# Kernel tuning notes

Hardware: AMD Instinct MI355X
Metric: run time of the kernel (lower is better)

## Reference

```python
import jax, jax.numpy as jnp
import numpy as np

B, T, CIN, CH, M, NCLS = 2048, 8, 2048, 1024, 32, 21
EPS = 1e-8  # torch.cosine_similarity eps


def setup_inputs() -> dict:
    key = jax.random.key(0)
    ks = jax.random.split(key, 16)
    g = lambda k, shp, sc=0.02: jax.random.normal(k, shp, dtype=jnp.float32) * sc
    return {
        "x": g(ks[0], (B, T, CIN), 1.0),
        "static_feat": g(ks[1], (NCLS, CIN, M), 1.0),  # 21 kmeans exemplar banks
        "Wk": g(ks[2], (CH, CIN)), "bk": g(ks[3], (CH,)),
        "Wv": g(ks[4], (CH, CIN)), "bv": g(ks[5], (CH,)),
        "WEk": g(ks[6], (CH, CIN)), "bEk": g(ks[7], (CH,)),
        "WEv": g(ks[8], (CH, CIN)), "bEv": g(ks[9], (CH,)),
        "Ww": g(ks[10], (1, CH)), "bw": g(ks[11], (1,)),
        "Wout": g(ks[12], (NCLS, 2 * CH)), "bout": g(ks[13], (NCLS,)),
    }


def reference(x, static_feat, Wk, bk, Wv, bv, WEk, bEk, WEv, bEv, Ww, bw, Wout, bout):
    # last frame only: [B, CIN]
    xl = x[:, -1, :]
    # 1x1 convs on length-1 sequence == dense projections
    k = xl @ Wk.T + bk          # [B, CH]
    v = xl @ Wv.T + bv          # [B, CH]
    # project all 21 static memories at once: [NCLS, CH, M]
    Ek = jnp.einsum('oc,ncm->nom', WEk, static_feat) + bEk[None, :, None]
    Ev = jnp.einsum('oc,ncm->nom', WEv, static_feat) + bEv[None, :, None]
    # cosine similarity along channel dim (torch clamps each norm at eps)
    kn = k / jnp.maximum(jnp.linalg.norm(k, axis=1, keepdims=True), EPS)
    Ekn = Ek / jnp.maximum(jnp.linalg.norm(Ek, axis=1, keepdims=True), EPS)
    cos = jnp.einsum('bo,nom->bnm', kn, Ekn)      # [B, NCLS, M]
    w = jax.nn.softmax(cos, axis=-1)               # softmax over exemplars
    s = jnp.einsum('nom,bnm->bno', Ev, w)          # weighted sums [B, NCLS, CH]
    # per-class scalar weights via conv2_1_W, softmax over the 21 classes
    fw = jax.nn.softmax(s @ Ww[0] + bw[0], axis=-1)  # [B, NCLS]
    fE = jnp.einsum('bno,bn->bo', s, fw)             # [B, CH]
    h = jax.nn.relu(jnp.concatenate([v, fE], axis=-1))  # [B, 2*CH]
    out = h @ Wout.T + bout                              # [B, NCLS]
    return out[:, :, None]  # [B, NCLS, 1] to match Conv1d output
```

## Files before the change

### kernel.cpp

```cpp
#include <hip/hip_runtime.h>
#include <math.h>

#define B_    2048
#define T_    8
#define CIN_  2048
#define CH_   1024
#define M_    32
#define NCLS_ 21
#define NM_   (NCLS_*M_)
#define NMP_  768
#define EPS_  1e-8f
#define ZKV_  4
#define ZC_   2

typedef __bf16 bf16_t;
typedef bf16_t bf16x4 __attribute__((ext_vector_type(4)));
typedef bf16_t bf16x8 __attribute__((ext_vector_type(8)));
typedef float  floatx4 __attribute__((ext_vector_type(4)));

#define GLOBAL_AS __attribute__((address_space(1)))
#define LDS_AS    __attribute__((address_space(3)))

__global__ __launch_bounds__(256) void gemm128(
    const bf16_t* __restrict__ A0, const bf16_t* __restrict__ A1, int msplit,
    const bf16_t* __restrict__ B0, const bf16_t* __restrict__ B1,
    const float* __restrict__ bias0, const float* __restrict__ bias1,
    int ld, float* __restrict__ C, int ldc, size_t strideC, int mzero, int Ksplit)
{
  __shared__ bf16_t As[128 * 64];
  __shared__ bf16_t Bs[128 * 64];
  const int tid = threadIdx.x;
  const int n0 = blockIdx.x * 128, m0 = blockIdx.y * 128;
  const int z = blockIdx.z;

  const bf16_t* A; const bf16_t* B; const float* bias; int mrow;
  if (m0 < msplit) { A = A0; B = B0; bias = bias0; mrow = m0; }
  else             { A = A1; B = B1; bias = bias1; mrow = m0 - msplit; }
  const int koff = z * Ksplit;

  const int w = tid >> 6, lane = tid & 63;
  const int srow = lane >> 3;
  const int sblk = (lane & 7) ^ srow;
  const bf16_t* ga = A + (size_t)(mrow + w * 32 + srow) * ld + koff + sblk * 8;
  const bf16_t* gb = B + (size_t)(n0   + w * 32 + srow) * ld + koff + sblk * 8;

  const int wm = (w >> 1) * 64, wn = (w & 1) * 64;
  const int l15 = lane & 15, quad = lane >> 4;
  const int sx = l15 & 7;

  floatx4 acc[4][4] = {};

  for (int k0 = 0; k0 < Ksplit; k0 += 64) {
    __syncthreads();
    #pragma unroll
    for (int q = 0; q < 4; ++q) {
      __builtin_amdgcn_global_load_lds(
          (const GLOBAL_AS void*)(ga + (size_t)q * 8 * ld),
          (LDS_AS void*)(&As[(w * 4 + q) * 512]), 16, 0, 0);
      __builtin_amdgcn_global_load_lds(
          (const GLOBAL_AS void*)(gb + (size_t)q * 8 * ld),
          (LDS_AS void*)(&Bs[(w * 4 + q) * 512]), 16, 0, 0);
    }
    ga += 64; gb += 64;
    __syncthreads();
    #pragma unroll
    for (int ks = 0; ks < 2; ++ks) {
      bf16x8 af[4], bfr[4];
      #pragma unroll
      for (int i = 0; i < 4; ++i)
        af[i] = *(const bf16x8*)(&As[(wm + i * 16 + l15) * 64 + ((ks * 4 + quad) ^ sx) * 8]);
      #pragma unroll
      for (int j = 0; j < 4; ++j)
        bfr[j] = *(const bf16x8*)(&Bs[(wn + j * 16 + l15) * 64 + ((ks * 4 + quad) ^ sx) * 8]);
      #pragma unroll
      for (int i = 0; i < 4; ++i)
        #pragma unroll
        for (int j = 0; j < 4; ++j)
          acc[i][j] = __builtin_amdgcn_mfma_f32_16x16x32_bf16(af[i], bfr[j], acc[i][j], 0, 0, 0);
    }
  }

  float* Cz = C + (size_t)z * strideC;
  #pragma unroll
  for (int i = 0; i < 4; ++i) {
    const int rbase = m0 + wm + i * 16 + quad * 4;
    #pragma unroll
    for (int j = 0; j < 4; ++j) {
      const int c = n0 + wn + j * 16 + l15;
      const float badd = (bias && z == 0) ? bias[c] : 0.f;
      #pragma unroll
      for (int r = 0; r < 4; ++r) {
        const int rr = rbase + r;
        float v = acc[i][j][r] + badd;
        if (rr >= mzero) v = 0.f;
        Cz[(size_t)rr * ldc + c] = v;
      }
    }
  }
}

template<int MODE>
__global__ __launch_bounds__(256) void gemm_n64(
    const bf16_t* __restrict__ A, const bf16_t* __restrict__ B, int ld,
    float* __restrict__ C, bf16_t* __restrict__ Cb, int ldc, size_t strideC,
    int Ksplit)
{
  __shared__ bf16_t As[128 * 64];
  __shared__ bf16_t Bs[64 * 64];
  const int tid = threadIdx.x;
  const int n0 = blockIdx.x * 64, m0 = blockIdx.y * 128;
  const int z = blockIdx.z;
  const int koff = z * Ksplit;

  const int w = tid >> 6, lane = tid & 63;
  const int srow = lane >> 3;
  const int sblk = (lane & 7) ^ srow;
  const bf16_t* ga = A + (size_t)(m0 + w * 32 + srow) * ld + koff + sblk * 8;
  const bf16_t* gb = B + (size_t)(n0 + w * 16 + srow) * ld + koff + sblk * 8;

  const int l15 = lane & 15, quad = lane >> 4;
  const int sx = l15 & 7;

  floatx4 acc[2][4] = {};

  for (int k0 = 0; k0 < Ksplit; k0 += 64) {
    __syncthreads();
    #pragma unroll
    for (int q = 0; q < 4; ++q)
      __builtin_amdgcn_global_load_lds(
          (const GLOBAL_AS void*)(ga + (size_t)q * 8 * ld),
          (LDS_AS void*)(&As[(w * 4 + q) * 512]), 16, 0, 0);
    #pragma unroll
    for (int q = 0; q < 2; ++q)
      __builtin_amdgcn_global_load_lds(
          (const GLOBAL_AS void*)(gb + (size_t)q * 8 * ld),
          (LDS_AS void*)(&Bs[(w * 2 + q) * 512]), 16, 0, 0);
    ga += 64; gb += 64;
    __syncthreads();
    #pragma unroll
    for (int ks = 0; ks < 2; ++ks) {
      bf16x8 af[2], bfr[4];
      #pragma unroll
      for (int i = 0; i < 2; ++i)
        af[i] = *(const bf16x8*)(&As[(w * 32 + i * 16 + l15) * 64 + ((ks * 4 + quad) ^ sx) * 8]);
      #pragma unroll
      for (int j = 0; j < 4; ++j)
        bfr[j] = *(const bf16x8*)(&Bs[(j * 16 + l15) * 64 + ((ks * 4 + quad) ^ sx) * 8]);
      #pragma unroll
      for (int i = 0; i < 2; ++i)
        #pragma unroll
        for (int j = 0; j < 4; ++j)
          acc[i][j] = __builtin_amdgcn_mfma_f32_16x16x32_bf16(af[i], bfr[j], acc[i][j], 0, 0, 0);
    }
  }

  #pragma unroll
  for (int i = 0; i < 2; ++i) {
    const int rbase = m0 + w * 32 + i * 16 + quad * 4;
    #pragma unroll
    for (int j = 0; j < 4; ++j) {
      const int c = n0 + j * 16 + l15;
      #pragma unroll
      for (int r = 0; r < 4; ++r) {
        const int rr = rbase + r;
        if (MODE == 0)
          (C + (size_t)z * strideC)[(size_t)rr * ldc + c] = acc[i][j][r];
        else
          Cb[(size_t)rr * ldc + c] = (bf16_t)fmaxf(acc[i][j][r], 0.f);
      }
    }
  }
}

__global__ __launch_bounds__(256) void kPrepAll(
    const float* __restrict__ x, const float* __restrict__ Wk,
    const float* __restrict__ Wv, const float* __restrict__ WEk,
    const float* __restrict__ WEv, const float* __restrict__ bk,
    const float* __restrict__ bv, const float* __restrict__ bEk,
    const float* __restrict__ bEv, const float* __restrict__ Wout,
    const float* __restrict__ sf,
    bf16_t* __restrict__ xb, bf16_t* __restrict__ Wkvb, bf16_t* __restrict__ WEb,
    bf16_t* __restrict__ Woutb, bf16_t* __restrict__ sfTb,
    float* __restrict__ bkv, float* __restrict__ bE)
{
  __shared__ float t[32][33];
  const int blk = blockIdx.x;
  const int tid = threadIdx.x;

  if (blk >= 3084) {
    const int tt = blk - 3084;
    const int nn = tt % 24;
    const int c0 = (tt / 24) * 32;
    const int cc = tid & 31, r8 = tid >> 5;
    #pragma unroll
    for (int q = 0; q < 4; ++q) {
      const int cl = r8 + q * 8;
      float v = 0.f;
      if (nn < NCLS_) v = sf[((size_t)nn * CIN_ + c0 + cl) * M_ + cc];
      t[cl][cc] = v;
    }
    __syncthreads();
    #pragma unroll
    for (int q = 0; q < 4; ++q) {
      const int ml = r8 + q * 8;
      sfTb[(size_t)(nn * 32 + ml) * CIN_ + c0 + cc] = (bf16_t)t[cc][ml];
    }
    return;
  }
  if (blk == 3072) {
    for (int i = tid; i < CH_; i += 256) {
      bkv[i] = bk[i]; bkv[CH_ + i] = bv[i];
      bE[i]  = bEk[i]; bE[CH_ + i] = bEv[i];
    }
    return;
  }
  if (blk > 3072) {
    const size_t e0 = ((size_t)(blk - 3073) * 256 + tid) * 16;
    if (e0 < (size_t)NCLS_ * 2 * CH_) {
      #pragma unroll
      for (int q = 0; q < 4; ++q) {
        const float4 v = *(const float4*)(Wout + e0 + q * 4);
        bf16x4 o = { (bf16_t)v.x, (bf16_t)v.y, (bf16_t)v.z, (bf16_t)v.w };
        *(bf16x4*)(Woutb + e0 + q * 4) = o;
      }
    }
    return;
  }
  const int sec = blk >> 10;
  const int tt = ((blk & 1023) << 8) + tid;
  const size_t e0 = (size_t)tt * 16;
  const int row = (int)(e0 >> 11);
  const int col = (int)(e0 & 2047);
  const float* src;
  bf16_t* dst;
  if (sec == 0) {
    src = x + (size_t)row * (T_ * CIN_) + (size_t)(T_ - 1) * CIN_ + col;
    dst = xb + e0;
  } else if (sec == 1) {
    src = (row < CH_ ? Wk + (size_t)row * CIN_ : Wv + (size_t)(row - CH_) * CIN_) + col;
    dst = Wkvb + e0;
  } else {
    src = (row < CH_ ? WEk + (size_t)row * CIN_ : WEv + (size_t)(row - CH_) * CIN_) + col;
    dst = WEb + e0;
  }
  #pragma unroll
  for (int q = 0; q < 4; ++q) {
    const float4 v = *(const float4*)(src + q * 4);
    bf16x4 o = { (bf16_t)v.x, (bf16_t)v.y, (bf16_t)v.z, (bf16_t)v.w };
    *(bf16x4*)(dst + q * 4) = o;
  }
}

__global__ __launch_bounds__(256) void kNormTr(
    const float* __restrict__ KVE, size_t PS, const float* __restrict__ Ww,
    bf16_t* __restrict__ knb, bf16_t* __restrict__ Eknb, float* __restrict__ EvW,
    bf16_t* __restrict__ Ev2b)
{
  __shared__ float t[32][33];
  const int blk = blockIdx.x;
  const int tid = threadIdx.x;

  if (blk < 704) {
    const int r = blk * 4 + (tid >> 6);
    const int lane = tid & 63;
    const float* row = KVE + (size_t)r * 2048;
    float vals[16];
    float ss = 0.f;
    #pragma unroll
    for (int i = 0; i < 16; ++i) {
      const int o = lane + i * 64;
      float v = row[o];
      #pragma unroll
      for (int z = 1; z < ZKV_; ++z) v += row[(size_t)z * PS + o];
      vals[i] = v;
      ss += v * v;
    }
    for (int off = 32; off; off >>= 1) ss += __shfl_xor(ss, off);
    const float inv = 1.f / fmaxf(sqrtf(ss), EPS_);
    bf16_t* dst = (r < B_) ? knb + (size_t)r * CH_ : Eknb + (size_t)(r - B_) * CH_;
    #pragma unroll
    for (int i = 0; i < 16; ++i) dst[lane + i * 64] = (bf16_t)(vals[i] * inv);
    if (r >= B_) {
      float dd = 0.f;
      for (int o = lane; o < CH_; o += 64) {
        float v = row[CH_ + o];
        #pragma unroll
        for (int z = 1; z < ZKV_; ++z) v += row[(size_t)z * PS + CH_ + o];
        dd += v * Ww[o];
      }
      for (int off = 32; off; off >>= 1) dd += __shfl_xor(dd, off);
      if (lane == 0) EvW[r - B_] = dd;
    }
    return;
  }
  const int tt = blk - 704;
  const int nm0 = (tt % 24) * 32;
  const int o0 = (tt / 24) * 32;
  const int cc = tid & 31, r8 = tid >> 5;
  #pragma unroll
  for (int q = 0; q < 4; ++q) {
    const int r = r8 + q * 8;
    const size_t idx = (size_t)(B_ + nm0 + r) * 2048 + CH_ + o0 + cc;
    float v = KVE[idx];
    #pragma unroll
    for (int z = 1; z < ZKV_; ++z) v += KVE[(size_t)z * PS + idx];
    t[r][cc] = v;
  }
  __syncthreads();
  #pragma unroll
  for (int q = 0; q < 4; ++q) {
    const int r = r8 + q * 8;
    Ev2b[(size_t)(o0 + r) * NMP_ + nm0 + cc] = (bf16_t)t[cc][r];
  }
}

__global__ __launch_bounds__(256) void kSoftmax(
    const float* __restrict__ cosb, size_t PSc,
    const float* __restrict__ EvW, const float* __restrict__ bw,
    bf16_t* __restrict__ wwb)
{
  const int b = blockIdx.x;
  const int tid = threadIdx.x;
  __shared__ float sc[NM_];
  __shared__ float sl[NCLS_];
  for (int i = tid; i < NM_; i += 256) {
    float v = cosb[(size_t)b * NMP_ + i];
    #pragma unroll
    for (int z = 1; z < ZC_; ++z) v += cosb[(size_t)z * PSc + (size_t)b * NMP_ + i];
    sc[i] = v;
  }
  __syncthreads();
  if (tid < NCLS_) {
    const int base = tid * M_;
    float mx = -1e30f;
    for (int m = 0; m < M_; ++m) mx = fmaxf(mx, sc[base + m]);
    float s = 0.f;
    for (int m = 0; m < M_; ++m) {
      const float e = __expf(sc[base + m] - mx);
      sc[base + m] = e;
      s += e;
    }
    const float inv = 1.f / s;
    float lg = 0.f;
    for (int m = 0; m < M_; ++m) {
      const float w = sc[base + m] * inv;
      sc[base + m] = w;
      lg += w * EvW[base + m];
    }
    sl[tid] = lg + bw[0];
  }
  __syncthreads();
  if (tid == 0) {
    float mx = -1e30f;
    for (int n = 0; n < NCLS_; ++n) mx = fmaxf(mx, sl[n]);
    float s = 0.f;
    for (int n = 0; n < NCLS_; ++n) { const float e = __expf(sl[n] - mx); sl[n] = e; s += e; }
    const float inv = 1.f / s;
    for (int n = 0; n < NCLS_; ++n) sl[n] *= inv;
  }
  __syncthreads();
  for (int i = tid; i < NMP_; i += 256) {
    const float v = (i < NM_) ? sc[i] * sl[i >> 5] : 0.f;
    wwb[(size_t)b * NMP_ + i] = (bf16_t)v;
  }
}

__global__ __launch_bounds__(256) void kOut(
    const float* __restrict__ KVE, size_t PS,
    const bf16_t* __restrict__ fEb, const bf16_t* __restrict__ Woutb,
    const float* __restrict__ bout, float* __restrict__ out)
{
  const int b = blockIdx.x;
  const int tid = threadIdx.x;
  __shared__ float h[2 * CH_];
  for (int j = tid; j < CH_; j += 256) {
    const size_t idx = (size_t)b * 2048 + CH_ + j;
    float v = KVE[idx];
    #pragma unroll
    for (int z = 1; z < ZKV_; ++z) v += KVE[(size_t)z * PS + idx];
    h[j] = fmaxf(v, 0.f);
  }
  for (int j = tid; j < CH_; j += 256)
    h[CH_ + j] = (float)fEb[(size_t)b * CH_ + j];
  __syncthreads();
  const int wave = tid >> 6, lane = tid & 63;
  for (int n = wave; n < NCLS_; n += 4) {
    const bf16_t* wr = Woutb + (size_t)n * (2 * CH_);
    float s = 0.f;
    for (int j = lane; j < 2 * CH_; j += 64) s += h[j] * (float)wr[j];
    for (int off = 32; off; off >>= 1) s += __shfl_xor(s, off);
    if (lane == 0) out[(size_t)b * NCLS_ + n] = s + bout[n];
  }
}

extern "C" void kernel_launch(void* const* d_in, const int* in_sizes, int n_in,
                              void* d_out, int out_size, void* d_ws, size_t ws_size,
                              hipStream_t stream)
{
  const float* x    = (const float*)d_in[0];
  const float* sf   = (const float*)d_in[1];
  const float* Wk   = (const float*)d_in[2];
  const float* bk   = (const float*)d_in[3];
  const float* Wv   = (const float*)d_in[4];
  const float* bv   = (const float*)d_in[5];
  const float* WEk  = (const float*)d_in[6];
  const float* bEk  = (const float*)d_in[7];
  const float* WEv  = (const float*)d_in[8];
  const float* bEv  = (const float*)d_in[9];
  const float* Ww   = (const float*)d_in[10];
  const float* bw   = (const float*)d_in[11];
  const float* Wout = (const float*)d_in[12];
  const float* bout = (const float*)d_in[13];
  float* out = (float*)d_out;

  char* ws = (char*)d_ws;
  size_t off = 0;
  auto alloc = [&](size_t bytes) { char* p = ws + off; off += (bytes + 255) & ~(size_t)255; return p; };
  const size_t PS  = (size_t)2816 * 2048;
  const size_t PSc = (size_t)B_ * NMP_;
  float*  KVE   = (float*)alloc(PS * ZKV_ * 4);
  bf16_t* xb    = (bf16_t*)alloc((size_t)2048 * 2048 * 2);
  bf16_t* Wkvb  = (bf16_t*)alloc((size_t)2048 * 2048 * 2);
  bf16_t* WEb   = (bf16_t*)alloc((size_t)2048 * 2048 * 2);
  bf16_t* sfTb  = (bf16_t*)alloc((size_t)NMP_ * 2048 * 2);
  bf16_t* knb   = (bf16_t*)alloc((size_t)B_ * CH_ * 2);
  bf16_t* Eknb  = (bf16_t*)alloc((size_t)NMP_ * CH_ * 2);
  bf16_t* Ev2b  = (bf16_t*)alloc((size_t)CH_ * NMP_ * 2);
  float*  cosb  = (float*)alloc(PSc * ZC_ * 4);
  bf16_t* wwb   = (bf16_t*)alloc((size_t)B_ * NMP_ * 2);
  bf16_t* fEb   = (bf16_t*)alloc((size_t)B_ * CH_ * 2);
  bf16_t* Woutb = (bf16_t*)alloc((size_t)NCLS_ * 2 * CH_ * 2);
  float*  bkv   = (float*)alloc(2 * CH_ * 4);
  float*  bE    = (float*)alloc(2 * CH_ * 4);
  float*  EvW   = (float*)alloc(NMP_ * 4);

  kPrepAll<<<4620, 256, 0, stream>>>(x, Wk, Wv, WEk, WEv, bk, bv, bEk, bEv,
                                     Wout, sf, xb, Wkvb, WEb, Woutb, sfTb,
                                     bkv, bE);
  gemm128<<<dim3(16, 22, ZKV_), 256, 0, stream>>>(
      xb, sfTb, B_, Wkvb, WEb, bkv, bE, CIN_,
      KVE, 2048, PS, B_ + NM_, CIN_ / ZKV_);
  kNormTr<<<1472, 256, 0, stream>>>(KVE, PS, Ww, knb, Eknb, EvW, Ev2b);
  gemm_n64<0><<<dim3(NMP_ / 64, 16, ZC_), 256, 0, stream>>>(
      knb, Eknb, CH_, cosb, nullptr, NMP_, PSc, CH_ / ZC_);
  kSoftmax<<<B_, 256, 0, stream>>>(cosb, PSc, EvW, bw, wwb);
  gemm_n64<1><<<dim3(CH_ / 64, 16, 1), 256, 0, stream>>>(
      wwb, Ev2b, NMP_, nullptr, fEb, CH_, 0, NMP_);
  kOut<<<B_, 256, 0, stream>>>(KVE, PS, fEb, Woutb, bout, out);
}
```

Measured before the change: 369.9 us.

## Store split-K partials in bf16 and halve KV split-K factor

The split-K partial outputs of the projection GEMM and the cosine GEMM are now written as bf16 instead of fp32, and the projection GEMM's split factor drops from 4 to 2. Downstream kernels (norm, softmax, output) read and sum the bf16 partials in fp32. This is meant to cut intermediate memory traffic for the large KVE and cos buffers by roughly 4x and 2x. The cost is fewer blocks in the first GEMM, which has less parallelism, plus rounding error in the partial sums, including the cosine logits before softmax.

```diff
diff --git a/kernel.cpp b/kernel.cpp
--- a/kernel.cpp
+++ b/kernel.cpp
@@ -10,7 +10,7 @@
 #define NM_   (NCLS_*M_)
 #define NMP_  768
 #define EPS_  1e-8f
-#define ZKV_  4
+#define ZKV_  2
 #define ZC_   2
 
 typedef __bf16 bf16_t;
@@ -25,7 +25,7 @@
     const bf16_t* __restrict__ A0, const bf16_t* __restrict__ A1, int msplit,
     const bf16_t* __restrict__ B0, const bf16_t* __restrict__ B1,
     const float* __restrict__ bias0, const float* __restrict__ bias1,
-    int ld, float* __restrict__ C, int ldc, size_t strideC, int mzero, int Ksplit)
+    int ld, bf16_t* __restrict__ C, int ldc, size_t strideC, int mzero, int Ksplit)
 {
   __shared__ bf16_t As[128 * 64];
   __shared__ bf16_t Bs[128 * 64];
@@ -80,7 +80,7 @@
     }
   }
 
-  float* Cz = C + (size_t)z * strideC;
+  bf16_t* Cz = C + (size_t)z * strideC;
   #pragma unroll
   for (int i = 0; i < 4; ++i) {
     const int rbase = m0 + wm + i * 16 + quad * 4;
@@ -93,7 +93,7 @@
         const int rr = rbase + r;
         float v = acc[i][j][r] + badd;
         if (rr >= mzero) v = 0.f;
-        Cz[(size_t)rr * ldc + c] = v;
+        Cz[(size_t)rr * ldc + c] = (bf16_t)v;
       }
     }
   }
@@ -102,8 +102,7 @@
 template<int MODE>
 __global__ __launch_bounds__(256) void gemm_n64(
     const bf16_t* __restrict__ A, const bf16_t* __restrict__ B, int ld,
-    float* __restrict__ C, bf16_t* __restrict__ Cb, int ldc, size_t strideC,
-    int Ksplit)
+    bf16_t* __restrict__ Cb, int ldc, size_t strideC, int Ksplit)
 {
   __shared__ bf16_t As[128 * 64];
   __shared__ bf16_t Bs[64 * 64];
@@ -154,6 +153,7 @@
     }
   }
 
+  bf16_t* Cz = Cb + (size_t)z * strideC;
   #pragma unroll
   for (int i = 0; i < 2; ++i) {
     const int rbase = m0 + w * 32 + i * 16 + quad * 4;
@@ -163,10 +163,8 @@
       #pragma unroll
       for (int r = 0; r < 4; ++r) {
         const int rr = rbase + r;
-        if (MODE == 0)
-          (C + (size_t)z * strideC)[(size_t)rr * ldc + c] = acc[i][j][r];
-        else
-          Cb[(size_t)rr * ldc + c] = (bf16_t)fmaxf(acc[i][j][r], 0.f);
+        const float v = acc[i][j][r];
+        Cz[(size_t)rr * ldc + c] = (bf16_t)(MODE == 1 ? fmaxf(v, 0.f) : v);
       }
     }
   }
@@ -252,7 +250,7 @@
 }
 
 __global__ __launch_bounds__(256) void kNormTr(
-    const float* __restrict__ KVE, size_t PS, const float* __restrict__ Ww,
+    const bf16_t* __restrict__ KVE, size_t PS, const float* __restrict__ Ww,
     bf16_t* __restrict__ knb, bf16_t* __restrict__ Eknb, float* __restrict__ EvW,
     bf16_t* __restrict__ Ev2b)
 {
@@ -263,15 +261,15 @@
   if (blk < 704) {
     const int r = blk * 4 + (tid >> 6);
     const int lane = tid & 63;
-    const float* row = KVE + (size_t)r * 2048;
+    const bf16_t* row = KVE + (size_t)r * 2048;
     float vals[16];
     float ss = 0.f;
     #pragma unroll
     for (int i = 0; i < 16; ++i) {
       const int o = lane + i * 64;
-      float v = row[o];
-      #pragma unroll
-      for (int z = 1; z < ZKV_; ++z) v += row[(size_t)z * PS + o];
+      float v = (float)row[o];
+      #pragma unroll
+      for (int z = 1; z < ZKV_; ++z) v += (float)row[(size_t)z * PS + o];
       vals[i] = v;
       ss += v * v;
     }
@@ -283,9 +281,9 @@
     if (r >= B_) {
       float dd = 0.f;
       for (int o = lane; o < CH_; o += 64) {
-        float v = row[CH_ + o];
+        float v = (float)row[CH_ + o];
         #pragma unroll
-        for (int z = 1; z < ZKV_; ++z) v += row[(size_t)z * PS + CH_ + o];
+        for (int z = 1; z < ZKV_; ++z) v += (float)row[(size_t)z * PS + CH_ + o];
         dd += v * Ww[o];
       }
       for (int off = 32; off; off >>= 1) dd += __shfl_xor(dd, off);
@@ -301,9 +299,9 @@
   for (int q = 0; q < 4; ++q) {
     const int r = r8 + q * 8;
     const size_t idx = (size_t)(B_ + nm0 + r) * 2048 + CH_ + o0 + cc;
-    float v = KVE[idx];
-    #pragma unroll
-    for (int z = 1; z < ZKV_; ++z) v += KVE[(size_t)z * PS + idx];
+    float v = (float)KVE[idx];
+    #pragma unroll
+    for (int z = 1; z < ZKV_; ++z) v += (float)KVE[(size_t)z * PS + idx];
     t[r][cc] = v;
   }
   __syncthreads();
@@ -315,7 +313,7 @@
 }
 
 __global__ __launch_bounds__(256) void kSoftmax(
-    const float* __restrict__ cosb, size_t PSc,
+    const bf16_t* __restrict__ cosb, size_t PSc,
     const float* __restrict__ EvW, const float* __restrict__ bw,
     bf16_t* __restrict__ wwb)
 {
@@ -324,9 +322,9 @@
   __shared__ float sc[NM_];
   __shared__ float sl[NCLS_];
   for (int i = tid; i < NM_; i += 256) {
-    float v = cosb[(size_t)b * NMP_ + i];
-    #pragma unroll
-    for (int z = 1; z < ZC_; ++z) v += cosb[(size_t)z * PSc + (size_t)b * NMP_ + i];
+    float v = (float)cosb[(size_t)b * NMP_ + i];
+    #pragma unroll
+    for (int z = 1; z < ZC_; ++z) v += (float)cosb[(size_t)z * PSc + (size_t)b * NMP_ + i];
     sc[i] = v;
   }
   __syncthreads();
@@ -366,7 +364,7 @@
 }
 
 __global__ __launch_bounds__(256) void kOut(
-    const float* __restrict__ KVE, size_t PS,
+    const bf16_t* __restrict__ KVE, size_t PS,
     const bf16_t* __restrict__ fEb, const bf16_t* __restrict__ Woutb,
     const float* __restrict__ bout, float* __restrict__ out)
 {
@@ -375,9 +373,9 @@
   __shared__ float h[2 * CH_];
   for (int j = tid; j < CH_; j += 256) {
     const size_t idx = (size_t)b * 2048 + CH_ + j;
-    float v = KVE[idx];
-    #pragma unroll
-    for (int z = 1; z < ZKV_; ++z) v += KVE[(size_t)z * PS + idx];
+    float v = (float)KVE[idx];
+    #pragma unroll
+    for (int z = 1; z < ZKV_; ++z) v += (float)KVE[(size_t)z * PS + idx];
     h[j] = fmaxf(v, 0.f);
   }
   for (int j = tid; j < CH_; j += 256)
@@ -418,7 +416,7 @@
   auto alloc = [&](size_t bytes) { char* p = ws + off; off += (bytes + 255) & ~(size_t)255; return p; };
   const size_t PS  = (size_t)2816 * 2048;
   const size_t PSc = (size_t)B_ * NMP_;
-  float*  KVE   = (float*)alloc(PS * ZKV_ * 4);
+  bf16_t* KVE   = (bf16_t*)alloc(PS * ZKV_ * 2);
   bf16_t* xb    = (bf16_t*)alloc((size_t)2048 * 2048 * 2);
   bf16_t* Wkvb  = (bf16_t*)alloc((size_t)2048 * 2048 * 2);
   bf16_t* WEb   = (bf16_t*)alloc((size_t)2048 * 2048 * 2);
@@ -426,7 +424,7 @@
   bf16_t* knb   = (bf16_t*)alloc((size_t)B_ * CH_ * 2);
   bf16_t* Eknb  = (bf16_t*)alloc((size_t)NMP_ * CH_ * 2);
   bf16_t* Ev2b  = (bf16_t*)alloc((size_t)CH_ * NMP_ * 2);
-  float*  cosb  = (float*)alloc(PSc * ZC_ * 4);
+  bf16_t* cosb  = (bf16_t*)alloc(PSc * ZC_ * 2);
   bf16_t* wwb   = (bf16_t*)alloc((size_t)B_ * NMP_ * 2);
   bf16_t* fEb   = (bf16_t*)alloc((size_t)B_ * CH_ * 2);
   bf16_t* Woutb = (bf16_t*)alloc((size_t)NCLS_ * 2 * CH_ * 2);
@@ -442,9 +440,9 @@
       KVE, 2048, PS, B_ + NM_, CIN_ / ZKV_);
   kNormTr<<<1472, 256, 0, stream>>>(KVE, PS, Ww, knb, Eknb, EvW, Ev2b);
   gemm_n64<0><<<dim3(NMP_ / 64, 16, ZC_), 256, 0, stream>>>(
-      knb, Eknb, CH_, cosb, nullptr, NMP_, PSc, CH_ / ZC_);
+      knb, Eknb, CH_, cosb, NMP_, PSc, CH_ / ZC_);
   kSoftmax<<<B_, 256, 0, stream>>>(cosb, PSc, EvW, bw, wwb);
   gemm_n64<1><<<dim3(CH_ / 64, 16, 1), 256, 0, stream>>>(
-      wwb, Ev2b, NMP_, nullptr, fEb, CH_, 0, NMP_);
+      wwb, Ev2b, NMP_, fEb, CH_, 0, NMP_);
   kOut<<<B_, 256, 0, stream>>>(KVE, PS, fEb, Woutb, bout, out);
 }
```

Measured after the change: 349.3 us. 1.06x faster.
